# Kernel optimization log

Hardware: AMD Instinct MI355X
Metric: run time of the kernel (lower is better)

Reference implementation:

```python
import jax, jax.numpy as jnp
import numpy as np

N0, R, ND = 500000, 100000, 50000
E0, E1 = 2000000, 1000000
NODE_DIM, REVIEW_DIM, FINAL_DIM, H = 64, 64, 32, 4


def setup_inputs() -> dict:
    key = jax.random.key(0)
    ks = jax.random.split(key, 12)
    x = jax.random.normal(ks[0], (N0, NODE_DIM), dtype=jnp.float32)
    norm_n = jax.random.uniform(ks[1], (N0,), dtype=jnp.float32)
    norm_e = jax.random.uniform(ks[2], (E0,), dtype=jnp.float32)
    W1 = jax.random.normal(ks[3], (NODE_DIM, REVIEW_DIM), dtype=jnp.float32) * 0.05
    b1 = jax.random.normal(ks[4], (REVIEW_DIM,), dtype=jnp.float32) * 0.05
    Wsrc = jax.random.normal(ks[5], (REVIEW_DIM, H * FINAL_DIM), dtype=jnp.float32) * 0.05
    bsrc = jax.random.normal(ks[6], (H * FINAL_DIM,), dtype=jnp.float32) * 0.05
    attn = jax.random.normal(ks[7], (H, FINAL_DIM), dtype=jnp.float32) * 0.05
    src0 = jax.random.randint(ks[8], (E0,), 0, N0, dtype=jnp.int32)
    dst0 = jax.random.randint(ks[9], (E0,), 0, N0, dtype=jnp.int32)
    # 5 nodes per review graph (batched-graph membership for dgl.mean_nodes)
    node_graph = (jnp.arange(N0, dtype=jnp.int32) // (N0 // R)).astype(jnp.int32)
    src1 = jax.random.randint(ks[10], (E1,), 0, R, dtype=jnp.int32)
    dst1 = jax.random.randint(ks[11], (E1,), 0, ND, dtype=jnp.int32)
    # guarantee every dst node has at least one incoming edge (no 0-in-degree)
    dst1 = dst1.at[:ND].set(jnp.arange(ND, dtype=jnp.int32))
    return {"x": x, "norm_n": norm_n, "norm_e": norm_e, "W1": W1, "b1": b1,
            "Wsrc": Wsrc, "bsrc": bsrc, "attn": attn,
            "src0": src0, "dst0": dst0, "node_graph": node_graph,
            "src1": src1, "dst1": dst1}


def _leaky(v, slope):
    return jnp.where(v >= 0, v, slope * v)


def _edge_softmax(score, dst, n):
    # numerically stable per-destination softmax over edges; score [E,H]
    m = jax.ops.segment_max(score, dst, num_segments=n)
    ex = jnp.exp(score - m[dst])
    s = jax.ops.segment_sum(ex, dst, num_segments=n)
    return ex / s[dst]


def reference(x, norm_n, norm_e, W1, b1, Wsrc, bsrc, attn,
              src0, dst0, node_graph, src1, dst1):
    # ---- HypergraphLayer (blocks[0]) ----
    coef = norm_n[src0] * norm_n[dst0] * norm_e            # [E0]
    m = x[src0] * coef[:, None]                            # [E0, D_in]
    h = jax.ops.segment_sum(m, dst0, num_segments=N0)      # [N0, D_in]
    cnt = jax.ops.segment_sum(jnp.ones((N0,), x.dtype), node_graph, num_segments=R)
    r = jax.ops.segment_sum(h, node_graph, num_segments=R) / cnt[:, None]  # mean_nodes -> [R, D_in]
    r = _leaky(r @ W1 + b1, 0.01)                          # [R, review_dim]
    # ---- HEARConv / GATv2 (blocks[1]); fc_dst frozen at zero => er = 0 ----
    feat_src = (r @ Wsrc + bsrc).reshape(R, H, FINAL_DIM)  # [R, H, D]
    el = feat_src[src1]                                    # [E1, H, D]
    e = _leaky(el, 0.2)
    score = jnp.einsum('ehd,hd->eh', e, attn)              # [E1, H]
    alpha = _edge_softmax(score, dst1, ND)                 # [E1, H]
    ft = jax.ops.segment_sum(el * alpha[..., None], dst1, num_segments=ND)  # [ND, H, D]
    return ft.sum(axis=1)                                  # [ND, final_dim]
```

## Files before the change

### kernel.cpp

```cpp
#include <hip/hip_runtime.h>
#include <hip/hip_fp16.h>
#include <math.h>

#define N0c 500000
#define Rc  100000
#define NDc 50000
#define E0c 2000000
#define E1c 1000000
#define GB0 64
#define NB0 1563
#define DB1 64
#define NB1 782
#define NBk (NB0 + NB1)
#define T0  3072
#define T1  1536
#define PB  652
#define CAP0 1792
#define CAP1 1792
#define MT2  128


__global__ __launch_bounds__(256) void k_convert(const float4* __restrict__ x,
                                                 uint4* __restrict__ xh) {
    int i = blockIdx.x * 256 + threadIdx.x;
    const int NT = (N0c * 64) / 8;
    if (i < NT) {
        float4 a = x[2 * i], b = x[2 * i + 1];
        __half2 h0 = __floats2half2_rn(a.x, a.y);
        __half2 h1 = __floats2half2_rn(a.z, a.w);
        __half2 h2 = __floats2half2_rn(b.x, b.y);
        __half2 h3 = __floats2half2_rn(b.z, b.w);
        uint4 o;
        o.x = *(unsigned*)&h0; o.y = *(unsigned*)&h1;
        o.z = *(unsigned*)&h2; o.w = *(unsigned*)&h3;
        xh[i] = o;
    }
}

__global__ __launch_bounds__(1024) void k_place(
        const int* __restrict__ src0, const int* __restrict__ dst0,
        const float* __restrict__ norm_n, const float* __restrict__ norm_e,
        const int* __restrict__ src1, const int* __restrict__ dst1,
        unsigned* __restrict__ gcur,
        int2* __restrict__ coarse0, int* __restrict__ coarse1) {
    __shared__ unsigned cnt_s[NBk];
    __shared__ unsigned lo_s[NBk + 1];
    __shared__ unsigned dst_s[NBk];
    __shared__ unsigned pack_e[T0 + T1];
    __shared__ unsigned pack_s[T0 + T1];
    __shared__ float    pc_s[T0];

    int tid = threadIdx.x, b = blockIdx.x;
    int base0 = b * T0, base1 = b * T1;

    for (int i = tid; i < NBk; i += 1024) cnt_s[i] = 0u;
    __syncthreads();

    for (int i = tid; i < T0; i += 1024) {
        int e = base0 + i;
        if (e < E0c) {
            int d = dst0[e];
            unsigned q5 = (unsigned)d / 5u;
            unsigned bk = q5 >> 6;
            atomicAdd(&cnt_s[bk], 1u);
            pack_e[i] = (unsigned)i | ((q5 & 63u) << 12) | (bk << 18);
            pc_s[i] = norm_n[d] * norm_e[e];
        }
    }
    for (int i = tid; i < T1; i += 1024) {
        int e = base1 + i;
        if (e < E1c) {
            int d = dst1[e];
            unsigned bkAll = NB0 + ((unsigned)d >> 6);
            atomicAdd(&cnt_s[bkAll], 1u);
            pack_e[T0 + i] = (unsigned)i | ((unsigned)(d & 63) << 12) | (bkAll << 18);
        }
    }
    __syncthreads();

    unsigned a0 = (3 * tid     < NBk) ? cnt_s[3 * tid]     : 0u;
    unsigned a1 = (3 * tid + 1 < NBk) ? cnt_s[3 * tid + 1] : 0u;
    unsigned a2 = (3 * tid + 2 < NBk) ? cnt_s[3 * tid + 2] : 0u;
    unsigned ssum = a0 + a1 + a2;
    unsigned* scratch = pack_s;
    scratch[tid] = ssum;
    __syncthreads();
    for (int off = 1; off < 1024; off <<= 1) {
        unsigned t = (tid >= off) ? scratch[tid - off] : 0u;
        __syncthreads();
        scratch[tid] += t;
        __syncthreads();
    }
    unsigned ex = scratch[tid] - ssum;
    if (3 * tid     < NBk) lo_s[3 * tid]     = ex;
    if (3 * tid + 1 < NBk) lo_s[3 * tid + 1] = ex + a0;
    if (3 * tid + 2 < NBk) lo_s[3 * tid + 2] = ex + a0 + a1;
    if (tid == 1023) lo_s[NBk] = scratch[1023];
    __syncthreads();

    for (int i = tid; i < NBk; i += 1024) {
        unsigned c = cnt_s[i];
        unsigned rb = c ? atomicAdd(&gcur[i], c) : 0u;
        unsigned sb = (i < NB0) ? (unsigned)i * CAP0 : (unsigned)(i - NB0) * CAP1;
        dst_s[i] = sb + rb - lo_s[i];
    }
    __syncthreads();
    for (int i = tid; i < NBk; i += 1024) cnt_s[i] = lo_s[i];
    __syncthreads();

    for (int i = tid; i < T0; i += 1024) {
        if (base0 + i < E0c) {
            unsigned pk = pack_e[i];
            unsigned slot = atomicAdd(&cnt_s[pk >> 18], 1u);
            pack_s[slot] = pk;
        }
    }
    for (int i = tid; i < T1; i += 1024) {
        if (base1 + i < E1c) {
            unsigned pk = pack_e[T0 + i];
            unsigned slot = atomicAdd(&cnt_s[pk >> 18], 1u);
            pack_s[slot] = pk;
        }
    }
    __syncthreads();

    unsigned ntot = lo_s[NBk];
    for (unsigned j = tid; j < ntot; j += 1024) {
        unsigned pk = pack_s[j];
        unsigned bkAll = pk >> 18;
        unsigned low = (pk >> 12) & 63u;
        unsigned i = pk & 4095u;
        unsigned idx = dst_s[bkAll] + j;
        if (bkAll < NB0) {
            if (idx - bkAll * CAP0 < CAP0) {
                int e = base0 + (int)i;
                int s = src0[e];
                float coef = pc_s[i] * norm_n[s];
                coarse0[idx] = make_int2(s | (int)(low << 19), __float_as_int(coef));
            }
        } else {
            if (idx - (bkAll - NB0) * CAP1 < CAP1) {
                int e = base1 + (int)i;
                coarse1[idx] = src1[e] | (int)(low << 17);
            }
        }
    }
}

__global__ __launch_bounds__(512) void k_bucket0(
        const __half* __restrict__ xh, const int2* __restrict__ coarse0,
        const unsigned* __restrict__ gcur, float* __restrict__ r_mean) {
    __shared__ unsigned cur_s[GB0];
    __shared__ unsigned off_s[GB0 + 1];
    __shared__ int2  raw_s[CAP0];
    __shared__ int   sa[CAP0];
    __shared__ float ca[CAP0];
    int B = blockIdx.x, tid = threadIdx.x;
    int g0 = B * GB0;
    int ng = min(GB0, Rc - g0);
    size_t beg = (size_t)B * CAP0;
    int n = min((int)gcur[B], CAP0);
    if (tid < GB0) cur_s[tid] = 0u;
    __syncthreads();
    for (int i = tid; i < n; i += 512) {
        int2 p = coarse0[beg + i];
        raw_s[i] = p;
        atomicAdd(&cur_s[(p.x >> 19) & 63], 1u);
    }
    __syncthreads();
    if (tid < 64) {
        unsigned c = cur_s[tid];
        unsigned sc = c;
        for (int o = 1; o < 64; o <<= 1) {
            unsigned t = __shfl_up(sc, o);
            if (tid >= o) sc += t;
        }
        off_s[tid] = sc - c;
        if (tid == 63) off_s[GB0] = sc;
    }
    __syncthreads();
    if (tid < GB0) cur_s[tid] = off_s[tid];
    __syncthreads();
    for (int i = tid; i < n; i += 512) {
        int2 p = raw_s[i];
        unsigned slot = atomicAdd(&cur_s[(p.x >> 19) & 63], 1u);
        sa[slot] = p.x & 0x7FFFF;
        ca[slot] = __int_as_float(p.y);
    }
    __syncthreads();
    int wav = tid >> 6, lane = tid & 63, q = lane >> 4, l = lane & 15;
    for (int g = wav; g < ng; g += 8) {
        int rbeg = (int)off_s[g], rend = (int)off_s[g + 1];
        float4 acc = {0.f, 0.f, 0.f, 0.f};
        for (int j0 = rbeg + q; j0 < rend; j0 += 16) {
            int j1 = j0 + 4, j2 = j0 + 8, j3 = j0 + 12;
            int s0 = sa[j0];                 float c0 = ca[j0];
            int s1 = 0; float c1 = 0.f;
            int s2 = 0; float c2 = 0.f;
            int s3 = 0; float c3 = 0.f;
            if (j1 < rend) { s1 = sa[j1]; c1 = ca[j1]; }
            if (j2 < rend) { s2 = sa[j2]; c2 = ca[j2]; }
            if (j3 < rend) { s3 = sa[j3]; c3 = ca[j3]; }
            uint2 u0 = ((const uint2*)(xh + (size_t)s0 * 64))[l];
            uint2 u1 = ((const uint2*)(xh + (size_t)s1 * 64))[l];
            uint2 u2 = ((const uint2*)(xh + (size_t)s2 * 64))[l];
            uint2 u3 = ((const uint2*)(xh + (size_t)s3 * 64))[l];
            float2 a0 = __half22float2(*(__half2*)&u0.x), b0 = __half22float2(*(__half2*)&u0.y);
            float2 a1 = __half22float2(*(__half2*)&u1.x), b1 = __half22float2(*(__half2*)&u1.y);
            float2 a2 = __half22float2(*(__half2*)&u2.x), b2 = __half22float2(*(__half2*)&u2.y);
            float2 a3 = __half22float2(*(__half2*)&u3.x), b3 = __half22float2(*(__half2*)&u3.y);
            acc.x += a0.x * c0 + a1.x * c1 + a2.x * c2 + a3.x * c3;
            acc.y += a0.y * c0 + a1.y * c1 + a2.y * c2 + a3.y * c3;
            acc.z += b0.x * c0 + b1.x * c1 + b2.x * c2 + b3.x * c3;
            acc.w += b0.y * c0 + b1.y * c1 + b2.y * c2 + b3.y * c3;
        }
        acc.x += __shfl_xor(acc.x, 16); acc.y += __shfl_xor(acc.y, 16);
        acc.z += __shfl_xor(acc.z, 16); acc.w += __shfl_xor(acc.w, 16);
        acc.x += __shfl_xor(acc.x, 32); acc.y += __shfl_xor(acc.y, 32);
        acc.z += __shfl_xor(acc.z, 32); acc.w += __shfl_xor(acc.w, 32);
        if (q == 0) {
            float4 o = {acc.x * 0.2f, acc.y * 0.2f, acc.z * 0.2f, acc.w * 0.2f};
            ((float4*)(r_mean + (size_t)(g0 + g) * 64))[l] = o;
        }
    }
}

__global__ __launch_bounds__(512) void k_mlp(const float* __restrict__ r_in,
                                             const float* __restrict__ W1,
                                             const float* __restrict__ b1,
                                             const float* __restrict__ Wsrc,
                                             const float* __restrict__ bsrc,
                                             const float* __restrict__ attn,
                                             __half* __restrict__ feat_h,
                                             float* __restrict__ score_src, int R) {
    __shared__ float W1s[64 * 64];
    __shared__ float Wss[64 * 128];
    __shared__ float b1s[64], bss[128], atts[128];
    __shared__ float in_s[MT2 * 68];
    __shared__ float t1_s[MT2 * 68];
    int tid = threadIdx.x;
    for (int i = tid; i < 4096; i += 512) W1s[i] = W1[i];
    for (int i = tid; i < 8192; i += 512) Wss[i] = Wsrc[i];
    if (tid < 64) b1s[tid] = b1[tid];
    if (tid >= 64 && tid < 192) bss[tid - 64] = bsrc[tid - 64];
    if (tid >= 192 && tid < 320) atts[tid - 192] = attn[tid - 192];

    size_t rbase = (size_t)blockIdx.x * MT2;
    for (int idx = tid; idx < MT2 * 16; idx += 512) {
        int row = idx >> 4, cc = idx & 15;
        size_t gr = rbase + row;
        float4 v = {0.f, 0.f, 0.f, 0.f};
        if (gr < (size_t)R) v = ((const float4*)(r_in + gr * 64))[cc];
        *((float4*)&in_s[row * 68 + cc * 4]) = v;
    }
    __syncthreads();

    int c = tid & 15, rg = tid >> 4;
    const float* inr = in_s + rg * 4 * 68;
    {
        float4 a0 = {0,0,0,0}, a1 = {0,0,0,0}, a2 = {0,0,0,0}, a3 = {0,0,0,0};
        const float* wcol = W1s + c * 4;
#pragma unroll 8
        for (int k = 0; k < 64; k++) {
            float4 w = *((const float4*)(wcol + k * 64));
            float i0 = inr[k], i1 = inr[68 + k], i2 = inr[136 + k], i3 = inr[204 + k];
            a0.x += i0 * w.x; a0.y += i0 * w.y; a0.z += i0 * w.z; a0.w += i0 * w.w;
            a1.x += i1 * w.x; a1.y += i1 * w.y; a1.z += i1 * w.z; a1.w += i1 * w.w;
            a2.x += i2 * w.x; a2.y += i2 * w.y; a2.z += i2 * w.z; a2.w += i2 * w.w;
            a3.x += i3 * w.x; a3.y += i3 * w.y; a3.z += i3 * w.z; a3.w += i3 * w.w;
        }
        const float4 bb = *((const float4*)(b1s + c * 4));
        float4 r[4] = {a0, a1, a2, a3};
#pragma unroll
        for (int j = 0; j < 4; j++) {
            float4 a = r[j];
            a.x += bb.x; a.y += bb.y; a.z += bb.z; a.w += bb.w;
            a.x = a.x >= 0.f ? a.x : 0.01f * a.x;
            a.y = a.y >= 0.f ? a.y : 0.01f * a.y;
            a.z = a.z >= 0.f ? a.z : 0.01f * a.z;
            a.w = a.w >= 0.f ? a.w : 0.01f * a.w;
            *((float4*)&t1_s[(rg * 4 + j) * 68 + c * 4]) = a;
        }
    }
    __syncthreads();

    {
        float4 p0[4], p1[4];
#pragma unroll
        for (int j = 0; j < 4; j++) { p0[j] = {0,0,0,0}; p1[j] = {0,0,0,0}; }
        const float* t1r = t1_s + rg * 4 * 68;
        const float* wA = Wss + c * 4;
        const float* wB = Wss + 64 + c * 4;
#pragma unroll 8
        for (int k = 0; k < 64; k++) {
            float4 w0 = *((const float4*)(wA + k * 128));
            float4 w1 = *((const float4*)(wB + k * 128));
            float t0 = t1r[k], t1v = t1r[68 + k], t2 = t1r[136 + k], t3 = t1r[204 + k];
            p0[0].x += t0 * w0.x; p0[0].y += t0 * w0.y; p0[0].z += t0 * w0.z; p0[0].w += t0 * w0.w;
            p1[0].x += t0 * w1.x; p1[0].y += t0 * w1.y; p1[0].z += t0 * w1.z; p1[0].w += t0 * w1.w;
            p0[1].x += t1v * w0.x; p0[1].y += t1v * w0.y; p0[1].z += t1v * w0.z; p0[1].w += t1v * w0.w;
            p1[1].x += t1v * w1.x; p1[1].y += t1v * w1.y; p1[1].z += t1v * w1.z; p1[1].w += t1v * w1.w;
            p0[2].x += t2 * w0.x; p0[2].y += t2 * w0.y; p0[2].z += t2 * w0.z; p0[2].w += t2 * w0.w;
            p1[2].x += t2 * w1.x; p1[2].y += t2 * w1.y; p1[2].z += t2 * w1.z; p1[2].w += t2 * w1.w;
            p0[3].x += t3 * w0.x; p0[3].y += t3 * w0.y; p0[3].z += t3 * w0.z; p0[3].w += t3 * w0.w;
            p1[3].x += t3 * w1.x; p1[3].y += t3 * w1.y; p1[3].z += t3 * w1.z; p1[3].w += t3 * w1.w;
        }
        const float4 bA = *((const float4*)(bss + c * 4));
        const float4 bB = *((const float4*)(bss + 64 + c * 4));
        const float4 atA = *((const float4*)(atts + c * 4));
        const float4 atB = *((const float4*)(atts + 64 + c * 4));
#pragma unroll
        for (int j = 0; j < 4; j++) {
            size_t grow = rbase + rg * 4 + j;
            float4 vA = p0[j], vB = p1[j];
            vA.x += bA.x; vA.y += bA.y; vA.z += bA.z; vA.w += bA.w;
            vB.x += bB.x; vB.y += bB.y; vB.z += bB.z; vB.w += bB.w;
            if (grow < (size_t)R) {
                __half2 h0 = __floats2half2_rn(vA.x, vA.y);
                __half2 h1 = __floats2half2_rn(vA.z, vA.w);
                __half2 h2 = __floats2half2_rn(vB.x, vB.y);
                __half2 h3 = __floats2half2_rn(vB.z, vB.w);
                uint2 wa, wb;
                wa.x = *(unsigned*)&h0; wa.y = *(unsigned*)&h1;
                wb.x = *(unsigned*)&h2; wb.y = *(unsigned*)&h3;
                *(uint2*)(feat_h + grow * 128 + c * 4) = wa;
                *(uint2*)(feat_h + grow * 128 + 64 + c * 4) = wb;
            }
            float pA =
                (vA.x >= 0.f ? vA.x : 0.2f * vA.x) * atA.x +
                (vA.y >= 0.f ? vA.y : 0.2f * vA.y) * atA.y +
                (vA.z >= 0.f ? vA.z : 0.2f * vA.z) * atA.z +
                (vA.w >= 0.f ? vA.w : 0.2f * vA.w) * atA.w;
            float pB =
                (vB.x >= 0.f ? vB.x : 0.2f * vB.x) * atB.x +
                (vB.y >= 0.f ? vB.y : 0.2f * vB.y) * atB.y +
                (vB.z >= 0.f ? vB.z : 0.2f * vB.z) * atB.z +
                (vB.w >= 0.f ? vB.w : 0.2f * vB.w) * atB.w;
            pA += __shfl_xor(pA, 1); pB += __shfl_xor(pB, 1);
            pA += __shfl_xor(pA, 2); pB += __shfl_xor(pB, 2);
            pA += __shfl_xor(pA, 4); pB += __shfl_xor(pB, 4);
            if ((c & 7) == 0 && grow < (size_t)R) {
                score_src[grow * 4 + (c >> 3)] = pA;
                score_src[grow * 4 + 2 + (c >> 3)] = pB;
            }
        }
    }
}

__global__ __launch_bounds__(512) void k_bucket1(
        const __half* __restrict__ feat_h, const float* __restrict__ score,
        const int* __restrict__ coarse1, const unsigned* __restrict__ gcur,
        float* __restrict__ out) {
    __shared__ unsigned cur_s[DB1];
    __shared__ unsigned off_s[DB1 + 1];
    __shared__ int raw_s[CAP1];
    __shared__ int sa[CAP1];
    int B = blockIdx.x, tid = threadIdx.x;
    int d0 = B * DB1;
    int nd = min(DB1, NDc - d0);
    size_t beg = (size_t)B * CAP1;
    int n = min((int)gcur[NB0 + B], CAP1);
    if (tid < DB1) cur_s[tid] = 0u;
    __syncthreads();
    for (int i = tid; i < n; i += 512) {
        int p = coarse1[beg + i];
        raw_s[i] = p;
        atomicAdd(&cur_s[(p >> 17) & 63], 1u);
    }
    __syncthreads();
    if (tid < 64) {
        unsigned c = cur_s[tid];
        unsigned sc = c;
        for (int o = 1; o < 64; o <<= 1) {
            unsigned t = __shfl_up(sc, o);
            if (tid >= o) sc += t;
        }
        off_s[tid] = sc - c;
        if (tid == 63) off_s[DB1] = sc;
    }
    __syncthreads();
    if (tid < DB1) cur_s[tid] = off_s[tid];
    __syncthreads();
    for (int i = tid; i < n; i += 512) {
        int p = raw_s[i];
        unsigned slot = atomicAdd(&cur_s[(p >> 17) & 63], 1u);
        sa[slot] = p & 0x1FFFF;
    }
    __syncthreads();
    int wav = tid >> 6, lane = tid & 63, q = lane >> 5, l = lane & 31, h = l >> 3;
    const float NEG = -3.0e38f;
    for (int dl = wav; dl < nd; dl += 8) {
        int rbeg = (int)off_s[dl], rend = (int)off_s[dl + 1];
        float4 mx = {NEG, NEG, NEG, NEG};
        for (int j = rbeg + lane; j < rend; j += 64) {
            int s = sa[j];
            float4 sc = ((const float4*)score)[s];
            mx.x = fmaxf(mx.x, sc.x); mx.y = fmaxf(mx.y, sc.y);
            mx.z = fmaxf(mx.z, sc.z); mx.w = fmaxf(mx.w, sc.w);
        }
#pragma unroll
        for (int o = 1; o < 64; o <<= 1) {
            mx.x = fmaxf(mx.x, __shfl_xor(mx.x, o));
            mx.y = fmaxf(mx.y, __shfl_xor(mx.y, o));
            mx.z = fmaxf(mx.z, __shfl_xor(mx.z, o));
            mx.w = fmaxf(mx.w, __shfl_xor(mx.w, o));
        }
        float mh = h == 0 ? mx.x : h == 1 ? mx.y : h == 2 ? mx.z : mx.w;
        float4 acc = {0.f, 0.f, 0.f, 0.f};
        float sex = 0.f;
        for (int j0 = rbeg + q; j0 < rend; j0 += 8) {
            int j1 = j0 + 2, j2 = j0 + 4, j3 = j0 + 6;
            int s0 = sa[j0];
            bool v1 = j1 < rend, v2 = j2 < rend, v3 = j3 < rend;
            int s1 = v1 ? sa[j1] : s0;
            int s2 = v2 ? sa[j2] : s0;
            int s3 = v3 ? sa[j3] : s0;
            float sc0 = score[4 * s0 + h];
            float sc1 = score[4 * s1 + h];
            float sc2 = score[4 * s2 + h];
            float sc3 = score[4 * s3 + h];
            uint2 u0 = ((const uint2*)(feat_h + (size_t)s0 * 128))[l];
            uint2 u1 = ((const uint2*)(feat_h + (size_t)s1 * 128))[l];
            uint2 u2 = ((const uint2*)(feat_h + (size_t)s2 * 128))[l];
            uint2 u3 = ((const uint2*)(feat_h + (size_t)s3 * 128))[l];
            float e0 = __expf(sc0 - mh);
            float e1 = v1 ? __expf(sc1 - mh) : 0.f;
            float e2 = v2 ? __expf(sc2 - mh) : 0.f;
            float e3 = v3 ? __expf(sc3 - mh) : 0.f;
            float2 f0a = __half22float2(*(__half2*)&u0.x), f0b = __half22float2(*(__half2*)&u0.y);
            float2 f1a = __half22float2(*(__half2*)&u1.x), f1b = __half22float2(*(__half2*)&u1.y);
            float2 f2a = __half22float2(*(__half2*)&u2.x), f2b = __half22float2(*(__half2*)&u2.y);
            float2 f3a = __half22float2(*(__half2*)&u3.x), f3b = __half22float2(*(__half2*)&u3.y);
            acc.x += f0a.x * e0 + f1a.x * e1 + f2a.x * e2 + f3a.x * e3;
            acc.y += f0a.y * e0 + f1a.y * e1 + f2a.y * e2 + f3a.y * e3;
            acc.z += f0b.x * e0 + f1b.x * e1 + f2b.x * e2 + f3b.x * e3;
            acc.w += f0b.y * e0 + f1b.y * e1 + f2b.y * e2 + f3b.y * e3;
            sex += e0 + e1 + e2 + e3;
        }
        acc.x += __shfl_xor(acc.x, 32); acc.y += __shfl_xor(acc.y, 32);
        acc.z += __shfl_xor(acc.z, 32); acc.w += __shfl_xor(acc.w, 32);
        sex += __shfl_xor(sex, 32);
        float inv = 1.f / sex;
        acc.x *= inv; acc.y *= inv; acc.z *= inv; acc.w *= inv;
        acc.x += __shfl_xor(acc.x, 8);  acc.y += __shfl_xor(acc.y, 8);
        acc.z += __shfl_xor(acc.z, 8);  acc.w += __shfl_xor(acc.w, 8);
        acc.x += __shfl_xor(acc.x, 16); acc.y += __shfl_xor(acc.y, 16);
        acc.z += __shfl_xor(acc.z, 16); acc.w += __shfl_xor(acc.w, 16);
        if (lane < 8) ((float4*)(out + (size_t)(d0 + dl) * 32))[lane] = acc;
    }
}

extern "C" void kernel_launch(void* const* d_in, const int* in_sizes, int n_in,
                              void* d_out, int out_size, void* d_ws, size_t ws_size,
                              hipStream_t stream) {
    const float* x      = (const float*)d_in[0];
    const float* norm_n = (const float*)d_in[1];
    const float* norm_e = (const float*)d_in[2];
    const float* W1     = (const float*)d_in[3];
    const float* b1     = (const float*)d_in[4];
    const float* Wsrc   = (const float*)d_in[5];
    const float* bsrc   = (const float*)d_in[6];
    const float* attn   = (const float*)d_in[7];
    const int* src0     = (const int*)d_in[8];
    const int* dst0     = (const int*)d_in[9];
    const int* src1     = (const int*)d_in[11];
    const int* dst1     = (const int*)d_in[12];
    float* out = (float*)d_out;

    char* ws = (char*)d_ws;
    size_t off = 0;
    auto alloc = [&](size_t bytes) {
        void* p = ws + off;
        off += (bytes + 255) & ~(size_t)255;
        return p;
    };

    unsigned* gcur = (unsigned*)alloc(NBk * 4);
    size_t zero_bytes = off;
    __half* xh = (__half*)alloc((size_t)N0c * 64 * 2);
    size_t regA = (size_t)Rc * 128 * 2;
    char* pA = (char*)alloc(regA);
    int2* coarse0  = (int2*)pA;
    __half* feat_h = (__half*)pA;
    int* coarse1  = (int*)alloc((size_t)NB1 * CAP1 * 4);
    float* r_mean = (float*)alloc((size_t)Rc * 64 * 4);
    float* score_src = (float*)alloc((size_t)Rc * 4 * 4);

    hipMemsetAsync(d_ws, 0, zero_bytes, stream);

    k_convert<<<(N0c * 64 / 8 + 255) / 256, 256, 0, stream>>>((const float4*)x, (uint4*)xh);
    k_place<<<PB, 1024, 0, stream>>>(src0, dst0, norm_n, norm_e,
                                     src1, dst1, gcur, coarse0, coarse1);

    k_bucket0<<<NB0, 512, 0, stream>>>(xh, coarse0, gcur, r_mean);
    k_mlp<<<(Rc + MT2 - 1) / MT2, 512, 0, stream>>>(r_mean, W1, b1, Wsrc, bsrc, attn,
                                                    feat_h, score_src, Rc);
    k_bucket1<<<NB1, 512, 0, stream>>>(feat_h, score_src, coarse1, gcur, out);
}
```

Baseline: 453.7 us.

## Fuse fp16 conversion of x into placement kernel and use wave-shuffle scan

Removes the separate k_convert launch and folds the float-to-half conversion of x into k_place, where each block converts a fixed chunk before doing its edge bucketing. This saves a launch and lets the streaming conversion overlap with the placement's atomic and scan work. The block-wide Hillis-Steele scan over bucket counts is replaced by a wave-level shuffle scan with a small cross-wave pass, cutting many barriers. The loop that copies lo_s into cnt_s is merged into the global-atomic loop, dropping one more sync. The trade-off is that k_place now carries the full 128 MB conversion traffic over only 652 blocks, so its runtime grows and the conversion may get less memory-level parallelism than the wide standalone launch had.

```diff
diff --git a/kernel.cpp b/kernel.cpp
--- a/kernel.cpp
+++ b/kernel.cpp
@@ -18,40 +18,45 @@
 #define CAP0 1792
 #define CAP1 1792
 #define MT2  128
-
-
-__global__ __launch_bounds__(256) void k_convert(const float4* __restrict__ x,
-                                                 uint4* __restrict__ xh) {
-    int i = blockIdx.x * 256 + threadIdx.x;
-    const int NT = (N0c * 64) / 8;
-    if (i < NT) {
-        float4 a = x[2 * i], b = x[2 * i + 1];
-        __half2 h0 = __floats2half2_rn(a.x, a.y);
-        __half2 h1 = __floats2half2_rn(a.z, a.w);
-        __half2 h2 = __floats2half2_rn(b.x, b.y);
-        __half2 h3 = __floats2half2_rn(b.z, b.w);
-        uint4 o;
-        o.x = *(unsigned*)&h0; o.y = *(unsigned*)&h1;
-        o.z = *(unsigned*)&h2; o.w = *(unsigned*)&h3;
-        xh[i] = o;
-    }
-}
+#define XCHUNK 6135
+
 
 __global__ __launch_bounds__(1024) void k_place(
         const int* __restrict__ src0, const int* __restrict__ dst0,
         const float* __restrict__ norm_n, const float* __restrict__ norm_e,
         const int* __restrict__ src1, const int* __restrict__ dst1,
         unsigned* __restrict__ gcur,
-        int2* __restrict__ coarse0, int* __restrict__ coarse1) {
+        int2* __restrict__ coarse0, int* __restrict__ coarse1,
+        const float4* __restrict__ x, uint4* __restrict__ xh) {
     __shared__ unsigned cnt_s[NBk];
     __shared__ unsigned lo_s[NBk + 1];
     __shared__ unsigned dst_s[NBk];
     __shared__ unsigned pack_e[T0 + T1];
     __shared__ unsigned pack_s[T0 + T1];
     __shared__ float    pc_s[T0];
+    __shared__ unsigned wsum[16];
 
     int tid = threadIdx.x, b = blockIdx.x;
     int base0 = b * T0, base1 = b * T1;
+
+    {
+        const int NT = (N0c * 64) / 8;
+        int cb = b * XCHUNK;
+        for (int i = tid; i < XCHUNK; i += 1024) {
+            int j = cb + i;
+            if (j < NT) {
+                float4 a = x[2 * j], c = x[2 * j + 1];
+                __half2 h0 = __floats2half2_rn(a.x, a.y);
+                __half2 h1 = __floats2half2_rn(a.z, a.w);
+                __half2 h2 = __floats2half2_rn(c.x, c.y);
+                __half2 h3 = __floats2half2_rn(c.z, c.w);
+                uint4 o;
+                o.x = *(unsigned*)&h0; o.y = *(unsigned*)&h1;
+                o.z = *(unsigned*)&h2; o.w = *(unsigned*)&h3;
+                xh[j] = o;
+            }
+        }
+    }
 
     for (int i = tid; i < NBk; i += 1024) cnt_s[i] = 0u;
     __syncthreads();
@@ -78,34 +83,47 @@
     }
     __syncthreads();
 
-    unsigned a0 = (3 * tid     < NBk) ? cnt_s[3 * tid]     : 0u;
-    unsigned a1 = (3 * tid + 1 < NBk) ? cnt_s[3 * tid + 1] : 0u;
-    unsigned a2 = (3 * tid + 2 < NBk) ? cnt_s[3 * tid + 2] : 0u;
-    unsigned ssum = a0 + a1 + a2;
-    unsigned* scratch = pack_s;
-    scratch[tid] = ssum;
-    __syncthreads();
-    for (int off = 1; off < 1024; off <<= 1) {
-        unsigned t = (tid >= off) ? scratch[tid - off] : 0u;
+    {
+        int lane = tid & 63, w = tid >> 6;
+        unsigned a0 = (3 * tid     < NBk) ? cnt_s[3 * tid]     : 0u;
+        unsigned a1 = (3 * tid + 1 < NBk) ? cnt_s[3 * tid + 1] : 0u;
+        unsigned a2 = (3 * tid + 2 < NBk) ? cnt_s[3 * tid + 2] : 0u;
+        unsigned s = a0 + a1 + a2;
+        unsigned sc = s;
+#pragma unroll
+        for (int o = 1; o < 64; o <<= 1) {
+            unsigned t = __shfl_up(sc, o);
+            if (lane >= o) sc += t;
+        }
+        if (lane == 63) wsum[w] = sc;
         __syncthreads();
-        scratch[tid] += t;
+        if (tid < 16) {
+            unsigned v = wsum[tid];
+            unsigned vs = v;
+#pragma unroll
+            for (int o = 1; o < 16; o <<= 1) {
+                unsigned t = __shfl_up(vs, o);
+                if (tid >= o) vs += t;
+            }
+            wsum[tid] = vs - v;
+            if (tid == 15) lo_s[NBk] = vs;
+        }
         __syncthreads();
-    }
-    unsigned ex = scratch[tid] - ssum;
-    if (3 * tid     < NBk) lo_s[3 * tid]     = ex;
-    if (3 * tid + 1 < NBk) lo_s[3 * tid + 1] = ex + a0;
-    if (3 * tid + 2 < NBk) lo_s[3 * tid + 2] = ex + a0 + a1;
-    if (tid == 1023) lo_s[NBk] = scratch[1023];
+        unsigned base = wsum[w] + (sc - s);
+        if (3 * tid     < NBk) lo_s[3 * tid]     = base;
+        if (3 * tid + 1 < NBk) lo_s[3 * tid + 1] = base + a0;
+        if (3 * tid + 2 < NBk) lo_s[3 * tid + 2] = base + a0 + a1;
+    }
     __syncthreads();
 
     for (int i = tid; i < NBk; i += 1024) {
         unsigned c = cnt_s[i];
+        unsigned lo = lo_s[i];
         unsigned rb = c ? atomicAdd(&gcur[i], c) : 0u;
         unsigned sb = (i < NB0) ? (unsigned)i * CAP0 : (unsigned)(i - NB0) * CAP1;
-        dst_s[i] = sb + rb - lo_s[i];
-    }
-    __syncthreads();
-    for (int i = tid; i < NBk; i += 1024) cnt_s[i] = lo_s[i];
+        dst_s[i] = sb + rb - lo;
+        cnt_s[i] = lo;
+    }
     __syncthreads();
 
     for (int i = tid; i < T0; i += 1024) {
@@ -488,9 +506,9 @@
 
     hipMemsetAsync(d_ws, 0, zero_bytes, stream);
 
-    k_convert<<<(N0c * 64 / 8 + 255) / 256, 256, 0, stream>>>((const float4*)x, (uint4*)xh);
     k_place<<<PB, 1024, 0, stream>>>(src0, dst0, norm_n, norm_e,
-                                     src1, dst1, gcur, coarse0, coarse1);
+                                     src1, dst1, gcur, coarse0, coarse1,
+                                     (const float4*)x, (uint4*)xh);
 
     k_bucket0<<<NB0, 512, 0, stream>>>(xh, coarse0, gcur, r_mean);
     k_mlp<<<(Rc + MT2 - 1) / MT2, 512, 0, stream>>>(r_mean, W1, b1, Wsrc, bsrc, attn,
```

Result: no change. 450.4 us (-0.7%).
